# Kernel tuning notes

Hardware: AMD Instinct MI355X
Metric: run time of the kernel (lower is better)

Reference implementation:

```python
import jax, jax.numpy as jnp
import numpy as np

HEADS = 8
EPS = 1e-5


def _layernorm(x, g, b):
    mu = jnp.mean(x, axis=-1, keepdims=True)
    var = jnp.mean(jnp.square(x - mu), axis=-1, keepdims=True)
    return (x - mu) * jax.lax.rsqrt(var + EPS) * g + b


def setup_inputs() -> dict:
    key = jax.random.key(0)
    ks = jax.random.split(key, 10)
    B, S, D = 4, 2048, 256
    d_ff = 2 * D
    s = 0.02
    return {
        "x": jax.random.normal(ks[0], (B, S, D), dtype=jnp.float32),
        "ln1_g": jnp.ones((D,), jnp.float32),
        "ln1_b": jnp.zeros((D,), jnp.float32),
        "w_qkv": jax.random.normal(ks[1], (3 * D, D), jnp.float32) * s,
        "b_qkv": jnp.zeros((3 * D,), jnp.float32),
        "w_proj": jax.random.normal(ks[2], (D, D), jnp.float32) * s,
        "b_proj": jnp.zeros((D,), jnp.float32),
        "ln2_g": jnp.ones((D,), jnp.float32),
        "ln2_b": jnp.zeros((D,), jnp.float32),
        "w1": jax.random.normal(ks[3], (d_ff, D), jnp.float32) * s,
        "b1": jnp.zeros((d_ff,), jnp.float32),
        "w2": jax.random.normal(ks[4], (D, d_ff), jnp.float32) * s,
        "b2": jnp.zeros((D,), jnp.float32),
    }


def reference(x, ln1_g, ln1_b, w_qkv, b_qkv, w_proj, b_proj,
              ln2_g, ln2_b, w1, b1, w2, b2):
    B, S, D = x.shape
    H = HEADS
    dh = D // H
    scale = dh ** -0.5

    # --- attention sublayer (pre-LN) ---
    y = _layernorm(x, ln1_g, ln1_b)
    qkv = y @ w_qkv.T + b_qkv                       # [B,S,3D]
    qkv = qkv.reshape(B, S, 3, H, dh)
    q = jnp.transpose(qkv[:, :, 0], (0, 2, 1, 3))   # [B,H,S,dh]
    k = jnp.transpose(qkv[:, :, 1], (0, 2, 1, 3))
    v = jnp.transpose(qkv[:, :, 2], (0, 2, 1, 3))
    attn = jax.nn.softmax(jnp.einsum('bhsd,bhtd->bhst', q, k) * scale, axis=-1)
    ctx = jnp.einsum('bhst,bhtd->bhsd', attn, v)    # [B,H,S,dh]
    ctx = jnp.transpose(ctx, (0, 2, 1, 3)).reshape(B, S, D)
    x = x + ctx @ w_proj.T + b_proj

    # --- FFN sublayer (pre-LN) ---
    y = _layernorm(x, ln2_g, ln2_b)
    h = jax.nn.silu(y @ w1.T + b1)                  # [B,S,2D]
    x = x + h @ w2.T + b2
    return x
```

## Files before the change

### kernel.cpp

```cpp
#include <hip/hip_runtime.h>
#include <cstddef>

constexpr int kB   = 4;
constexpr int kS   = 2048;
constexpr int kD   = 256;
constexpr int kH   = 8;
constexpr int kDH  = 32;
constexpr int kDFF = 512;
constexpr int kM   = kB * kS;
constexpr float kEps = 1e-5f;
constexpr float kScaleL2E = 0.17677669529663687f * 1.4426950408889634f;

typedef float f32x4  __attribute__((ext_vector_type(4)));
typedef short bf16x8 __attribute__((ext_vector_type(8)));
typedef unsigned short u16;
typedef unsigned int   u32;

__device__ inline u16 f2bf(float x) {
    union { float f; unsigned u; } c; c.f = x;
    const unsigned r = c.u + 0x7fffu + ((c.u >> 16) & 1u);
    return (u16)(r >> 16);
}

__device__ inline u32 pk_trunc(float lo, float hi) {
    union { float f; u32 u; } a, b; a.f = lo; b.f = hi;
    return __builtin_amdgcn_perm(b.u, a.u, 0x07060302u);
}

__global__ __launch_bounds__(256)
void ln_kernel(const float* __restrict__ x, const float* __restrict__ g,
               const float* __restrict__ b, u16* __restrict__ y)
{
    const int wave = threadIdx.x >> 6;
    const int lane = threadIdx.x & 63;
    const int row  = blockIdx.x * 4 + wave;
    const float4 v = *(const float4*)&x[(size_t)row * kD + lane * 4];
    float s1 = (v.x + v.y) + (v.z + v.w);
    float s2 = (v.x * v.x + v.y * v.y) + (v.z * v.z + v.w * v.w);
    #pragma unroll
    for (int off = 1; off < 64; off <<= 1) {
        s1 += __shfl_xor(s1, off);
        s2 += __shfl_xor(s2, off);
    }
    const float mu  = s1 * (1.0f / kD);
    const float var = s2 * (1.0f / kD) - mu * mu;
    const float inv = rsqrtf(var + kEps);
    const float4 g4 = *(const float4*)&g[lane * 4];
    const float4 b4 = *(const float4*)&b[lane * 4];
    *(ushort4*)&y[(size_t)row * kD + lane * 4] = make_ushort4(
        f2bf((v.x - mu) * inv * g4.x + b4.x),
        f2bf((v.y - mu) * inv * g4.y + b4.y),
        f2bf((v.z - mu) * inv * g4.z + b4.z),
        f2bf((v.w - mu) * inv * g4.w + b4.w));
}

template<int NT, int OUTMODE, bool RES, int KTOT>
__global__ __launch_bounds__(256)
void gemm_bf16(const u16* __restrict__ A, const float* __restrict__ Wf,
               const float* __restrict__ bias, const float* __restrict__ res,
               float* __restrict__ Cf, u16* __restrict__ Cb,
               u16* __restrict__ KbP, u16* __restrict__ VtP, int N)
{
    constexpr int BSTR = KTOT + 4;
    __shared__ u16 Bs[NT * BSTR];
    const int tid  = threadIdx.x;
    const int wave = tid >> 6;
    const int lane = tid & 63;
    const int quad = lane >> 4;
    const int l16  = lane & 15;
    const int m0 = blockIdx.x * 128;
    const int n0 = blockIdx.y * NT;

    {
        constexpr int ITS = (NT * KTOT) / 1024;
        #pragma unroll
        for (int it = 0; it < ITS; ++it) {
            const int e   = it * 1024 + tid * 4;
            const int row = e / KTOT;
            const int col = e & (KTOT - 1);
            const float4 wv = *(const float4*)&Wf[(size_t)(n0 + row) * KTOT + col];
            *(ushort4*)&Bs[row * BSTR + col] = make_ushort4(
                f2bf(wv.x), f2bf(wv.y), f2bf(wv.z), f2bf(wv.w));
        }
    }
    __syncthreads();

    f32x4 acc[2][NT / 16];
    #pragma unroll
    for (int mt = 0; mt < 2; ++mt)
        #pragma unroll
        for (int ni = 0; ni < NT / 16; ++ni) acc[mt][ni] = {0.f, 0.f, 0.f, 0.f};

    const u16* arow0 = &A[(size_t)(m0 + wave * 16 + l16) * KTOT];
    const u16* arow1 = &A[(size_t)(m0 + 64 + wave * 16 + l16) * KTOT];
    #pragma unroll 4
    for (int k0 = 0; k0 < KTOT; k0 += 32) {
        const bf16x8 a0 = *(const bf16x8*)&arow0[k0 + quad * 8];
        const bf16x8 a1 = *(const bf16x8*)&arow1[k0 + quad * 8];
        #pragma unroll
        for (int ni = 0; ni < NT / 16; ++ni) {
            const bf16x8 bf = *(const bf16x8*)&Bs[(ni * 16 + l16) * BSTR + k0 + quad * 8];
            acc[0][ni] = __builtin_amdgcn_mfma_f32_16x16x32_bf16(a0, bf, acc[0][ni], 0, 0, 0);
            acc[1][ni] = __builtin_amdgcn_mfma_f32_16x16x32_bf16(a1, bf, acc[1][ni], 0, 0, 0);
        }
    }

    #pragma unroll
    for (int mt = 0; mt < 2; ++mt) {
        #pragma unroll
        for (int ni = 0; ni < NT / 16; ++ni) {
            const float bias_v = bias[n0 + ni * 16 + l16];
            #pragma unroll
            for (int r = 0; r < 4; ++r) {
                const int m = m0 + mt * 64 + wave * 16 + quad * 4 + r;
                float v = acc[mt][ni][r] + bias_v;
                if (OUTMODE == 0) {
                    const int n = n0 + ni * 16 + l16;
                    if (RES) v += res[(size_t)m * N + n];
                    Cf[(size_t)m * N + n] = v;
                } else if (OUTMODE == 1) {
                    const int n = n0 + ni * 16 + l16;
                    v = v / (1.0f + __expf(-v));
                    Cb[(size_t)m * N + n] = f2bf(v);
                } else {
                    const int rgn = n0 >> 8;
                    const int nl  = (n0 & 255) + ni * 16 + l16;
                    const int hh  = nl >> 5, dh = nl & 31;
                    const int bb  = m >> 11, s = m & (kS - 1);
                    const int bh  = bb * kH + hh;
                    if (rgn == 0)
                        Cb[((size_t)bh * kS + s) * kDH + dh] = f2bf(v * kScaleL2E);
                    else if (rgn == 1)
                        KbP[((size_t)bh * kS + s) * kDH + dh] = f2bf(v);
                    else {
                        const int so = s & 31;
                        const int vq = (so >> 2) & 3;
                        const int vj = (so & 3) | (((so >> 4) & 1) << 2);
                        VtP[(((size_t)bh * (kS / 32) + (s >> 5)) * 4 + vq) * 256
                            + dh * 8 + vj] = f2bf(v);
                    }
                }
            }
        }
    }
}

__global__ __launch_bounds__(256)
void attn_kernel(const u16* __restrict__ Qb, const u16* __restrict__ Kb,
                 const u16* __restrict__ Vp, u16* __restrict__ ctx)
{
    __shared__ float cbuf[2][32 * 33];
    const int tid  = threadIdx.x;
    const int wave = tid >> 6;
    const int lane = tid & 63;
    const int quad = lane >> 4;
    const int l16  = lane & 15;
    const int h = blockIdx.y;
    const int b = blockIdx.z;
    const int bh = b * kH + h;
    const int qsub = wave >> 1;
    const int half = wave & 1;
    const int q0 = blockIdx.x * 64 + qsub * 32;

    bf16x8 aq[2];
    aq[0] = *(const bf16x8*)&Qb[((size_t)bh * kS + q0 + l16) * kDH + quad * 8];
    aq[1] = *(const bf16x8*)&Qb[((size_t)bh * kS + q0 + 16 + l16) * kDH + quad * 8];

    const u16* Kbase = Kb + (size_t)bh * kS * kDH;
    const u16* Vbase = Vp + (size_t)bh * (kS * 32);

    f32x4 O[2][2] = {};
    float lp[2] = {0.f, 0.f};
    const f32x4 zz = {0.f, 0.f, 0.f, 0.f};

    const int kbeg = half * (kS / 2);
    #pragma unroll 1
    for (int kt = kbeg; kt < kbeg + kS / 2; kt += 64) {
        bf16x8 kf[4];
        #pragma unroll
        for (int kg = 0; kg < 4; ++kg)
            kf[kg] = *(const bf16x8*)
                &Kbase[(size_t)(kt + kg * 16 + l16) * kDH + quad * 8];
        bf16x8 vf[2][2];
        #pragma unroll
        for (int ks = 0; ks < 2; ++ks)
            #pragma unroll
            for (int nf = 0; nf < 2; ++nf)
                vf[ks][nf] = *(const bf16x8*)
                    &Vbase[(size_t)(((kt >> 5) + ks) * 4 + quad) * 1024
                           + (nf * 16 + l16) * 8];

        #pragma unroll
        for (int qb = 0; qb < 2; ++qb) {
            f32x4 S[4];
            #pragma unroll
            for (int kg = 0; kg < 4; ++kg)
                S[kg] = __builtin_amdgcn_mfma_f32_16x16x32_bf16(kf[kg], aq[qb], zz, 0, 0, 0);

            float e0[8], e1[8];
            #pragma unroll
            for (int r = 0; r < 4; ++r) {
                e0[r]     = __builtin_amdgcn_exp2f(S[0][r]);
                e0[4 + r] = __builtin_amdgcn_exp2f(S[1][r]);
                e1[r]     = __builtin_amdgcn_exp2f(S[2][r]);
                e1[4 + r] = __builtin_amdgcn_exp2f(S[3][r]);
            }
            lp[qb] += ((e0[0] + e0[1]) + (e0[2] + e0[3]))
                    + ((e0[4] + e0[5]) + (e0[6] + e0[7]))
                    + ((e1[0] + e1[1]) + (e1[2] + e1[3]))
                    + ((e1[4] + e1[5]) + (e1[6] + e1[7]));
            union { u32 u[4]; bf16x8 v; } pA0, pA1;
            pA0.u[0] = pk_trunc(e0[0], e0[1]);
            pA0.u[1] = pk_trunc(e0[2], e0[3]);
            pA0.u[2] = pk_trunc(e0[4], e0[5]);
            pA0.u[3] = pk_trunc(e0[6], e0[7]);
            pA1.u[0] = pk_trunc(e1[0], e1[1]);
            pA1.u[1] = pk_trunc(e1[2], e1[3]);
            pA1.u[2] = pk_trunc(e1[4], e1[5]);
            pA1.u[3] = pk_trunc(e1[6], e1[7]);

            O[qb][0] = __builtin_amdgcn_mfma_f32_16x16x32_bf16(pA0.v, vf[0][0], O[qb][0], 0, 0, 0);
            O[qb][1] = __builtin_amdgcn_mfma_f32_16x16x32_bf16(pA0.v, vf[0][1], O[qb][1], 0, 0, 0);
            O[qb][0] = __builtin_amdgcn_mfma_f32_16x16x32_bf16(pA1.v, vf[1][0], O[qb][0], 0, 0, 0);
            O[qb][1] = __builtin_amdgcn_mfma_f32_16x16x32_bf16(pA1.v, vf[1][1], O[qb][1], 0, 0, 0);
        }
    }

    #pragma unroll
    for (int qb = 0; qb < 2; ++qb) {
        lp[qb] += __shfl_xor(lp[qb], 16);
        lp[qb] += __shfl_xor(lp[qb], 32);
    }

    float* cb = cbuf[qsub];
    if (half == 1) {
        #pragma unroll
        for (int qb = 0; qb < 2; ++qb)
            #pragma unroll
            for (int r = 0; r < 4; ++r) {
                const int row = qb * 16 + quad * 4 + r;
                cb[row * 33 + l16]      = O[qb][0][r];
                cb[row * 33 + 16 + l16] = O[qb][1][r];
                if (l16 == 0)
                    cb[row * 33 + 32] = __shfl(lp[qb], quad * 4 + r);
            }
    }
    __syncthreads();
    if (half == 0) {
        #pragma unroll
        for (int qb = 0; qb < 2; ++qb)
            #pragma unroll
            for (int r = 0; r < 4; ++r) {
                const int row = qb * 16 + quad * 4 + r;
                const float lq  = __shfl(lp[qb], quad * 4 + r) + cb[row * 33 + 32];
                const float inv = 1.0f / lq;
                const float o0 = O[qb][0][r] + cb[row * 33 + l16];
                const float o1 = O[qb][1][r] + cb[row * 33 + 16 + l16];
                const int q = q0 + row;
                u16* crow = ctx + ((size_t)(b * kS + q)) * kD + h * kDH;
                crow[l16]      = f2bf(o0 * inv);
                crow[16 + l16] = f2bf(o1 * inv);
            }
    }
}

extern "C" void kernel_launch(void* const* d_in, const int* in_sizes, int n_in,
                              void* d_out, int out_size, void* d_ws, size_t ws_size,
                              hipStream_t stream)
{
    const float* x      = (const float*)d_in[0];
    const float* ln1_g  = (const float*)d_in[1];
    const float* ln1_b  = (const float*)d_in[2];
    const float* w_qkv  = (const float*)d_in[3];
    const float* b_qkv  = (const float*)d_in[4];
    const float* w_proj = (const float*)d_in[5];
    const float* b_proj = (const float*)d_in[6];
    const float* ln2_g  = (const float*)d_in[7];
    const float* ln2_b  = (const float*)d_in[8];
    const float* w1     = (const float*)d_in[9];
    const float* b1     = (const float*)d_in[10];
    const float* w2     = (const float*)d_in[11];
    const float* b2     = (const float*)d_in[12];
    float* out = (float*)d_out;

    char* ws = (char*)d_ws;
    u16* Qb  = (u16*)ws;
    u16* Kb  = (u16*)(ws + ((size_t)4  << 20));
    u16* Vp  = (u16*)(ws + ((size_t)8  << 20));
    u16* ctx = (u16*)(ws + ((size_t)12 << 20));
    u16* y   = (u16*)(ws + ((size_t)16 << 20));
    u16* h   = (u16*)ws;

    const dim3 blk(256);

    ln_kernel<<<dim3(kM / 4), blk, 0, stream>>>(x, ln1_g, ln1_b, y);
    gemm_bf16<64, 2, false, 256><<<dim3(kM / 128, 12), blk, 0, stream>>>(
        y, w_qkv, b_qkv, nullptr, nullptr, Qb, Kb, Vp, 0);
    attn_kernel<<<dim3(kS / 64, kH, kB), blk, 0, stream>>>(Qb, Kb, Vp, ctx);
    gemm_bf16<32, 0, true, 256><<<dim3(kM / 128, kD / 32), blk, 0, stream>>>(
        ctx, w_proj, b_proj, x, out, nullptr, nullptr, nullptr, kD);
    ln_kernel<<<dim3(kM / 4), blk, 0, stream>>>(out, ln2_g, ln2_b, y);
    gemm_bf16<64, 1, false, 256><<<dim3(kM / 128, kDFF / 64), blk, 0, stream>>>(
        y, w1, b1, nullptr, nullptr, h, nullptr, nullptr, kDFF);
    gemm_bf16<32, 0, true, 512><<<dim3(kM / 128, kD / 32), blk, 0, stream>>>(
        h, w2, b2, out, out, nullptr, nullptr, nullptr, kD);
}
```

Baseline: 166.4 us.

## Fuse LayerNorm into the A-operand load of the QKV and FFN1 GEMMs

```diff
diff --git a/kernel.cpp b/kernel.cpp
--- a/kernel.cpp
+++ b/kernel.cpp
@@ -27,37 +27,12 @@
     return __builtin_amdgcn_perm(b.u, a.u, 0x07060302u);
 }
 
+template<int NT, int OUTMODE, bool RES, int KTOT, bool LNA>
 __global__ __launch_bounds__(256)
-void ln_kernel(const float* __restrict__ x, const float* __restrict__ g,
-               const float* __restrict__ b, u16* __restrict__ y)
-{
-    const int wave = threadIdx.x >> 6;
-    const int lane = threadIdx.x & 63;
-    const int row  = blockIdx.x * 4 + wave;
-    const float4 v = *(const float4*)&x[(size_t)row * kD + lane * 4];
-    float s1 = (v.x + v.y) + (v.z + v.w);
-    float s2 = (v.x * v.x + v.y * v.y) + (v.z * v.z + v.w * v.w);
-    #pragma unroll
-    for (int off = 1; off < 64; off <<= 1) {
-        s1 += __shfl_xor(s1, off);
-        s2 += __shfl_xor(s2, off);
-    }
-    const float mu  = s1 * (1.0f / kD);
-    const float var = s2 * (1.0f / kD) - mu * mu;
-    const float inv = rsqrtf(var + kEps);
-    const float4 g4 = *(const float4*)&g[lane * 4];
-    const float4 b4 = *(const float4*)&b[lane * 4];
-    *(ushort4*)&y[(size_t)row * kD + lane * 4] = make_ushort4(
-        f2bf((v.x - mu) * inv * g4.x + b4.x),
-        f2bf((v.y - mu) * inv * g4.y + b4.y),
-        f2bf((v.z - mu) * inv * g4.z + b4.z),
-        f2bf((v.w - mu) * inv * g4.w + b4.w));
-}
-
-template<int NT, int OUTMODE, bool RES, int KTOT>
-__global__ __launch_bounds__(256)
-void gemm_bf16(const u16* __restrict__ A, const float* __restrict__ Wf,
-               const float* __restrict__ bias, const float* __restrict__ res,
+void gemm_bf16(const void* __restrict__ Ain, const float* __restrict__ Wf,
+               const float* __restrict__ bias,
+               const float* __restrict__ lng, const float* __restrict__ lnb,
+               const float* __restrict__ res,
                float* __restrict__ Cf, u16* __restrict__ Cb,
                u16* __restrict__ KbP, u16* __restrict__ VtP, int N)
 {
@@ -83,6 +58,56 @@
                 f2bf(wv.x), f2bf(wv.y), f2bf(wv.z), f2bf(wv.w));
         }
     }
+
+    bf16x8 areg[2][LNA ? KTOT / 32 : 1];
+    if constexpr (LNA) {
+        static_assert(KTOT == 256, "LNA assumes K == D == 256");
+        const float* Af = (const float*)Ain;
+        #pragma unroll
+        for (int mt = 0; mt < 2; ++mt) {
+            const float* arow = &Af[(size_t)(m0 + mt * 64 + wave * 16 + l16) * kD];
+            float s1 = 0.f, s2 = 0.f;
+            #pragma unroll
+            for (int t = 0; t < 8; ++t) {
+                const float4 a0 = *(const float4*)&arow[t * 32 + quad * 8];
+                const float4 a1 = *(const float4*)&arow[t * 32 + quad * 8 + 4];
+                s1 += ((a0.x + a0.y) + (a0.z + a0.w))
+                    + ((a1.x + a1.y) + (a1.z + a1.w));
+                s2 = fmaf(a0.x, a0.x, s2); s2 = fmaf(a0.y, a0.y, s2);
+                s2 = fmaf(a0.z, a0.z, s2); s2 = fmaf(a0.w, a0.w, s2);
+                s2 = fmaf(a1.x, a1.x, s2); s2 = fmaf(a1.y, a1.y, s2);
+                s2 = fmaf(a1.z, a1.z, s2); s2 = fmaf(a1.w, a1.w, s2);
+            }
+            s1 += __shfl_xor(s1, 16); s1 += __shfl_xor(s1, 32);
+            s2 += __shfl_xor(s2, 16); s2 += __shfl_xor(s2, 32);
+            const float mu   = s1 * (1.0f / kD);
+            const float rsig = rsqrtf(s2 * (1.0f / kD) - mu * mu + kEps);
+            #pragma unroll
+            for (int t = 0; t < 8; ++t) {
+                const float4 a0 = *(const float4*)&arow[t * 32 + quad * 8];
+                const float4 a1 = *(const float4*)&arow[t * 32 + quad * 8 + 4];
+                const float4 g0 = *(const float4*)&lng[t * 32 + quad * 8];
+                const float4 g1 = *(const float4*)&lng[t * 32 + quad * 8 + 4];
+                const float4 b0 = *(const float4*)&lnb[t * 32 + quad * 8];
+                const float4 b1 = *(const float4*)&lnb[t * 32 + quad * 8 + 4];
+                float e[8];
+                e[0] = fmaf((a0.x - mu) * rsig, g0.x, b0.x);
+                e[1] = fmaf((a0.y - mu) * rsig, g0.y, b0.y);
+                e[2] = fmaf((a0.z - mu) * rsig, g0.z, b0.z);
+                e[3] = fmaf((a0.w - mu) * rsig, g0.w, b0.w);
+                e[4] = fmaf((a1.x - mu) * rsig, g1.x, b1.x);
+                e[5] = fmaf((a1.y - mu) * rsig, g1.y, b1.y);
+                e[6] = fmaf((a1.z - mu) * rsig, g1.z, b1.z);
+                e[7] = fmaf((a1.w - mu) * rsig, g1.w, b1.w);
+                union { u32 u[4]; bf16x8 v; } P;
+                P.u[0] = pk_trunc(e[0], e[1]);
+                P.u[1] = pk_trunc(e[2], e[3]);
+                P.u[2] = pk_trunc(e[4], e[5]);
+                P.u[3] = pk_trunc(e[6], e[7]);
+                areg[mt][t] = P.v;
+            }
+        }
+    }
     __syncthreads();
 
     f32x4 acc[2][NT / 16];
@@ -91,12 +116,18 @@
         #pragma unroll
         for (int ni = 0; ni < NT / 16; ++ni) acc[mt][ni] = {0.f, 0.f, 0.f, 0.f};
 
-    const u16* arow0 = &A[(size_t)(m0 + wave * 16 + l16) * KTOT];
-    const u16* arow1 = &A[(size_t)(m0 + 64 + wave * 16 + l16) * KTOT];
+    const u16* arow0 = LNA ? nullptr : &((const u16*)Ain)[(size_t)(m0 + wave * 16 + l16) * KTOT];
+    const u16* arow1 = LNA ? nullptr : &((const u16*)Ain)[(size_t)(m0 + 64 + wave * 16 + l16) * KTOT];
     #pragma unroll 4
     for (int k0 = 0; k0 < KTOT; k0 += 32) {
-        const bf16x8 a0 = *(const bf16x8*)&arow0[k0 + quad * 8];
-        const bf16x8 a1 = *(const bf16x8*)&arow1[k0 + quad * 8];
+        bf16x8 a0, a1;
+        if constexpr (LNA) {
+            a0 = areg[0][k0 / 32];
+            a1 = areg[1][k0 / 32];
+        } else {
+            a0 = *(const bf16x8*)&arow0[k0 + quad * 8];
+            a1 = *(const bf16x8*)&arow1[k0 + quad * 8];
+        }
         #pragma unroll
         for (int ni = 0; ni < NT / 16; ++ni) {
             const bf16x8 bf = *(const bf16x8*)&Bs[(ni * 16 + l16) * BSTR + k0 + quad * 8];
@@ -288,20 +319,21 @@
     u16* Kb  = (u16*)(ws + ((size_t)4  << 20));
     u16* Vp  = (u16*)(ws + ((size_t)8  << 20));
     u16* ctx = (u16*)(ws + ((size_t)12 << 20));
-    u16* y   = (u16*)(ws + ((size_t)16 << 20));
     u16* h   = (u16*)ws;
 
     const dim3 blk(256);
 
-    ln_kernel<<<dim3(kM / 4), blk, 0, stream>>>(x, ln1_g, ln1_b, y);
-    gemm_bf16<64, 2, false, 256><<<dim3(kM / 128, 12), blk, 0, stream>>>(
-        y, w_qkv, b_qkv, nullptr, nullptr, Qb, Kb, Vp, 0);
+    gemm_bf16<64, 2, false, 256, true><<<dim3(kM / 128, 12), blk, 0, stream>>>(
+        x, w_qkv, b_qkv, ln1_g, ln1_b, nullptr,
+        nullptr, Qb, Kb, Vp, 0);
     attn_kernel<<<dim3(kS / 64, kH, kB), blk, 0, stream>>>(Qb, Kb, Vp, ctx);
-    gemm_bf16<32, 0, true, 256><<<dim3(kM / 128, kD / 32), blk, 0, stream>>>(
-        ctx, w_proj, b_proj, x, out, nullptr, nullptr, nullptr, kD);
-    ln_kernel<<<dim3(kM / 4), blk, 0, stream>>>(out, ln2_g, ln2_b, y);
-    gemm_bf16<64, 1, false, 256><<<dim3(kM / 128, kDFF / 64), blk, 0, stream>>>(
-        y, w1, b1, nullptr, nullptr, h, nullptr, nullptr, kDFF);
-    gemm_bf16<32, 0, true, 512><<<dim3(kM / 128, kD / 32), blk, 0, stream>>>(
-        h, w2, b2, out, out, nullptr, nullptr, nullptr, kD);
-}
+    gemm_bf16<32, 0, true, 256, false><<<dim3(kM / 128, kD / 32), blk, 0, stream>>>(
+        ctx, w_proj, b_proj, nullptr, nullptr, x,
+        out, nullptr, nullptr, nullptr, kD);
+    gemm_bf16<64, 1, false, 256, true><<<dim3(kM / 128, kDFF / 64), blk, 0, stream>>>(
+        out, w1, b1, ln2_g, ln2_b, nullptr,
+        nullptr, h, nullptr, nullptr, kDFF);
+    gemm_bf16<32, 0, true, 512, false><<<dim3(kM / 128, kD / 32), blk, 0, stream>>>(
+        h, w2, b2, nullptr, nullptr, out,
+        out, nullptr, nullptr, nullptr, kD);
+}
```

After: 267.9 us. 1.61x slower.

## Load GEMM weights directly into registers instead of staging through LDS

Applied to the files above, without the earlier changes.

```diff
diff --git a/kernel.cpp b/kernel.cpp
--- a/kernel.cpp
+++ b/kernel.cpp
@@ -54,61 +54,58 @@
         f2bf((v.w - mu) * inv * g4.w + b4.w));
 }
 
-template<int NT, int OUTMODE, bool RES, int KTOT>
+template<int OUTMODE, bool RES, int KTOT>
 __global__ __launch_bounds__(256)
 void gemm_bf16(const u16* __restrict__ A, const float* __restrict__ Wf,
                const float* __restrict__ bias, const float* __restrict__ res,
                float* __restrict__ Cf, u16* __restrict__ Cb,
                u16* __restrict__ KbP, u16* __restrict__ VtP, int N)
 {
-    constexpr int BSTR = KTOT + 4;
-    __shared__ u16 Bs[NT * BSTR];
     const int tid  = threadIdx.x;
     const int wave = tid >> 6;
     const int lane = tid & 63;
     const int quad = lane >> 4;
     const int l16  = lane & 15;
     const int m0 = blockIdx.x * 128;
-    const int n0 = blockIdx.y * NT;
-
-    {
-        constexpr int ITS = (NT * KTOT) / 1024;
-        #pragma unroll
-        for (int it = 0; it < ITS; ++it) {
-            const int e   = it * 1024 + tid * 4;
-            const int row = e / KTOT;
-            const int col = e & (KTOT - 1);
-            const float4 wv = *(const float4*)&Wf[(size_t)(n0 + row) * KTOT + col];
-            *(ushort4*)&Bs[row * BSTR + col] = make_ushort4(
-                f2bf(wv.x), f2bf(wv.y), f2bf(wv.z), f2bf(wv.w));
-        }
-    }
-    __syncthreads();
-
-    f32x4 acc[2][NT / 16];
-    #pragma unroll
-    for (int mt = 0; mt < 2; ++mt)
-        #pragma unroll
-        for (int ni = 0; ni < NT / 16; ++ni) acc[mt][ni] = {0.f, 0.f, 0.f, 0.f};
+    const int n0 = blockIdx.y * 32;
+
+    f32x4 acc[2][2] = {};
 
     const u16* arow0 = &A[(size_t)(m0 + wave * 16 + l16) * KTOT];
     const u16* arow1 = &A[(size_t)(m0 + 64 + wave * 16 + l16) * KTOT];
-    #pragma unroll 4
-    for (int k0 = 0; k0 < KTOT; k0 += 32) {
-        const bf16x8 a0 = *(const bf16x8*)&arow0[k0 + quad * 8];
-        const bf16x8 a1 = *(const bf16x8*)&arow1[k0 + quad * 8];
-        #pragma unroll
-        for (int ni = 0; ni < NT / 16; ++ni) {
-            const bf16x8 bf = *(const bf16x8*)&Bs[(ni * 16 + l16) * BSTR + k0 + quad * 8];
-            acc[0][ni] = __builtin_amdgcn_mfma_f32_16x16x32_bf16(a0, bf, acc[0][ni], 0, 0, 0);
-            acc[1][ni] = __builtin_amdgcn_mfma_f32_16x16x32_bf16(a1, bf, acc[1][ni], 0, 0, 0);
+
+    #pragma unroll
+    for (int kc = 0; kc < KTOT; kc += 256) {
+        bf16x8 breg[2][8];
+        #pragma unroll
+        for (int ni = 0; ni < 2; ++ni) {
+            const float* wrow = &Wf[(size_t)(n0 + ni * 16 + l16) * KTOT + kc + quad * 8];
+            #pragma unroll
+            for (int t = 0; t < 8; ++t) {
+                const float4 w0 = *(const float4*)&wrow[t * 32];
+                const float4 w1 = *(const float4*)&wrow[t * 32 + 4];
+                union { ushort4 s[2]; bf16x8 v; } P;
+                P.s[0] = make_ushort4(f2bf(w0.x), f2bf(w0.y), f2bf(w0.z), f2bf(w0.w));
+                P.s[1] = make_ushort4(f2bf(w1.x), f2bf(w1.y), f2bf(w1.z), f2bf(w1.w));
+                breg[ni][t] = P.v;
+            }
+        }
+        #pragma unroll
+        for (int t = 0; t < 8; ++t) {
+            const int k0 = kc + t * 32;
+            const bf16x8 a0 = *(const bf16x8*)&arow0[k0 + quad * 8];
+            const bf16x8 a1 = *(const bf16x8*)&arow1[k0 + quad * 8];
+            acc[0][0] = __builtin_amdgcn_mfma_f32_16x16x32_bf16(a0, breg[0][t], acc[0][0], 0, 0, 0);
+            acc[1][0] = __builtin_amdgcn_mfma_f32_16x16x32_bf16(a1, breg[0][t], acc[1][0], 0, 0, 0);
+            acc[0][1] = __builtin_amdgcn_mfma_f32_16x16x32_bf16(a0, breg[1][t], acc[0][1], 0, 0, 0);
+            acc[1][1] = __builtin_amdgcn_mfma_f32_16x16x32_bf16(a1, breg[1][t], acc[1][1], 0, 0, 0);
         }
     }
 
     #pragma unroll
     for (int mt = 0; mt < 2; ++mt) {
         #pragma unroll
-        for (int ni = 0; ni < NT / 16; ++ni) {
+        for (int ni = 0; ni < 2; ++ni) {
             const float bias_v = bias[n0 + ni * 16 + l16];
             #pragma unroll
             for (int r = 0; r < 4; ++r) {
@@ -294,14 +291,14 @@
     const dim3 blk(256);
 
     ln_kernel<<<dim3(kM / 4), blk, 0, stream>>>(x, ln1_g, ln1_b, y);
-    gemm_bf16<64, 2, false, 256><<<dim3(kM / 128, 12), blk, 0, stream>>>(
+    gemm_bf16<2, false, 256><<<dim3(kM / 128, 24), blk, 0, stream>>>(
         y, w_qkv, b_qkv, nullptr, nullptr, Qb, Kb, Vp, 0);
     attn_kernel<<<dim3(kS / 64, kH, kB), blk, 0, stream>>>(Qb, Kb, Vp, ctx);
-    gemm_bf16<32, 0, true, 256><<<dim3(kM / 128, kD / 32), blk, 0, stream>>>(
+    gemm_bf16<0, true, 256><<<dim3(kM / 128, kD / 32), blk, 0, stream>>>(
         ctx, w_proj, b_proj, x, out, nullptr, nullptr, nullptr, kD);
     ln_kernel<<<dim3(kM / 4), blk, 0, stream>>>(out, ln2_g, ln2_b, y);
-    gemm_bf16<64, 1, false, 256><<<dim3(kM / 128, kDFF / 64), blk, 0, stream>>>(
+    gemm_bf16<1, false, 256><<<dim3(kM / 128, kDFF / 32), blk, 0, stream>>>(
         y, w1, b1, nullptr, nullptr, h, nullptr, nullptr, kDFF);
-    gemm_bf16<32, 0, true, 512><<<dim3(kM / 128, kD / 32), blk, 0, stream>>>(
+    gemm_bf16<0, true, 512><<<dim3(kM / 128, kD / 32), blk, 0, stream>>>(
         h, w2, b2, out, out, nullptr, nullptr, nullptr, kD);
 }
```

Result: slower. 216.3 us (+30.0%).

## Retile GEMMs to 256x32 blocks and compute softmax row sums via MFMA

Applied to the files above, without the earlier changes.

```diff
diff --git a/kernel.cpp b/kernel.cpp
--- a/kernel.cpp
+++ b/kernel.cpp
@@ -54,7 +54,7 @@
         f2bf((v.w - mu) * inv * g4.w + b4.w));
 }
 
-template<int NT, int OUTMODE, bool RES, int KTOT>
+template<int OUTMODE, bool RES, int KTOT>
 __global__ __launch_bounds__(256)
 void gemm_bf16(const u16* __restrict__ A, const float* __restrict__ Wf,
                const float* __restrict__ bias, const float* __restrict__ res,
@@ -62,17 +62,17 @@
                u16* __restrict__ KbP, u16* __restrict__ VtP, int N)
 {
     constexpr int BSTR = KTOT + 4;
-    __shared__ u16 Bs[NT * BSTR];
+    __shared__ u16 Bs[32 * BSTR];
     const int tid  = threadIdx.x;
     const int wave = tid >> 6;
     const int lane = tid & 63;
     const int quad = lane >> 4;
     const int l16  = lane & 15;
-    const int m0 = blockIdx.x * 128;
-    const int n0 = blockIdx.y * NT;
+    const int m0 = blockIdx.x * 256;
+    const int n0 = blockIdx.y * 32;
 
     {
-        constexpr int ITS = (NT * KTOT) / 1024;
+        constexpr int ITS = (32 * KTOT) / 1024;
         #pragma unroll
         for (int it = 0; it < ITS; ++it) {
             const int e   = it * 1024 + tid * 4;
@@ -85,30 +85,29 @@
     }
     __syncthreads();
 
-    f32x4 acc[2][NT / 16];
+    f32x4 acc[4][2] = {};
+
+    const u16* arow[4];
     #pragma unroll
-    for (int mt = 0; mt < 2; ++mt)
-        #pragma unroll
-        for (int ni = 0; ni < NT / 16; ++ni) acc[mt][ni] = {0.f, 0.f, 0.f, 0.f};
-
-    const u16* arow0 = &A[(size_t)(m0 + wave * 16 + l16) * KTOT];
-    const u16* arow1 = &A[(size_t)(m0 + 64 + wave * 16 + l16) * KTOT];
+    for (int mt = 0; mt < 4; ++mt)
+        arow[mt] = &A[(size_t)(m0 + mt * 64 + wave * 16 + l16) * KTOT];
+
     #pragma unroll 4
     for (int k0 = 0; k0 < KTOT; k0 += 32) {
-        const bf16x8 a0 = *(const bf16x8*)&arow0[k0 + quad * 8];
-        const bf16x8 a1 = *(const bf16x8*)&arow1[k0 + quad * 8];
-        #pragma unroll
-        for (int ni = 0; ni < NT / 16; ++ni) {
-            const bf16x8 bf = *(const bf16x8*)&Bs[(ni * 16 + l16) * BSTR + k0 + quad * 8];
-            acc[0][ni] = __builtin_amdgcn_mfma_f32_16x16x32_bf16(a0, bf, acc[0][ni], 0, 0, 0);
-            acc[1][ni] = __builtin_amdgcn_mfma_f32_16x16x32_bf16(a1, bf, acc[1][ni], 0, 0, 0);
+        const bf16x8 b0 = *(const bf16x8*)&Bs[l16 * BSTR + k0 + quad * 8];
+        const bf16x8 b1 = *(const bf16x8*)&Bs[(16 + l16) * BSTR + k0 + quad * 8];
+        #pragma unroll
+        for (int mt = 0; mt < 4; ++mt) {
+            const bf16x8 a = *(const bf16x8*)&arow[mt][k0 + quad * 8];
+            acc[mt][0] = __builtin_amdgcn_mfma_f32_16x16x32_bf16(a, b0, acc[mt][0], 0, 0, 0);
+            acc[mt][1] = __builtin_amdgcn_mfma_f32_16x16x32_bf16(a, b1, acc[mt][1], 0, 0, 0);
         }
     }
 
     #pragma unroll
-    for (int mt = 0; mt < 2; ++mt) {
-        #pragma unroll
-        for (int ni = 0; ni < NT / 16; ++ni) {
+    for (int mt = 0; mt < 4; ++mt) {
+        #pragma unroll
+        for (int ni = 0; ni < 2; ++ni) {
             const float bias_v = bias[n0 + ni * 16 + l16];
             #pragma unroll
             for (int r = 0; r < 4; ++r) {
@@ -169,8 +168,12 @@
     const u16* Kbase = Kb + (size_t)bh * kS * kDH;
     const u16* Vbase = Vp + (size_t)bh * (kS * 32);
 
+    bf16x8 ones;
+    #pragma unroll
+    for (int i = 0; i < 8; ++i) ones[i] = (short)0x3F80;
+
     f32x4 O[2][2] = {};
-    float lp[2] = {0.f, 0.f};
+    f32x4 lacc[2] = {};
     const f32x4 zz = {0.f, 0.f, 0.f, 0.f};
 
     const int kbeg = half * (kS / 2);
@@ -205,10 +208,6 @@
                 e1[r]     = __builtin_amdgcn_exp2f(S[2][r]);
                 e1[4 + r] = __builtin_amdgcn_exp2f(S[3][r]);
             }
-            lp[qb] += ((e0[0] + e0[1]) + (e0[2] + e0[3]))
-                    + ((e0[4] + e0[5]) + (e0[6] + e0[7]))
-                    + ((e1[0] + e1[1]) + (e1[2] + e1[3]))
-                    + ((e1[4] + e1[5]) + (e1[6] + e1[7]));
             union { u32 u[4]; bf16x8 v; } pA0, pA1;
             pA0.u[0] = pk_trunc(e0[0], e0[1]);
             pA0.u[1] = pk_trunc(e0[2], e0[3]);
@@ -221,15 +220,11 @@
 
             O[qb][0] = __builtin_amdgcn_mfma_f32_16x16x32_bf16(pA0.v, vf[0][0], O[qb][0], 0, 0, 0);
             O[qb][1] = __builtin_amdgcn_mfma_f32_16x16x32_bf16(pA0.v, vf[0][1], O[qb][1], 0, 0, 0);
+            lacc[qb] = __builtin_amdgcn_mfma_f32_16x16x32_bf16(pA0.v, ones, lacc[qb], 0, 0, 0);
             O[qb][0] = __builtin_amdgcn_mfma_f32_16x16x32_bf16(pA1.v, vf[1][0], O[qb][0], 0, 0, 0);
             O[qb][1] = __builtin_amdgcn_mfma_f32_16x16x32_bf16(pA1.v, vf[1][1], O[qb][1], 0, 0, 0);
+            lacc[qb] = __builtin_amdgcn_mfma_f32_16x16x32_bf16(pA1.v, ones, lacc[qb], 0, 0, 0);
         }
-    }
-
-    #pragma unroll
-    for (int qb = 0; qb < 2; ++qb) {
-        lp[qb] += __shfl_xor(lp[qb], 16);
-        lp[qb] += __shfl_xor(lp[qb], 32);
     }
 
     float* cb = cbuf[qsub];
@@ -241,8 +236,7 @@
                 const int row = qb * 16 + quad * 4 + r;
                 cb[row * 33 + l16]      = O[qb][0][r];
                 cb[row * 33 + 16 + l16] = O[qb][1][r];
-                if (l16 == 0)
-                    cb[row * 33 + 32] = __shfl(lp[qb], quad * 4 + r);
+                if (l16 == 0) cb[row * 33 + 32] = lacc[qb][r];
             }
     }
     __syncthreads();
@@ -252,7 +246,7 @@
             #pragma unroll
             for (int r = 0; r < 4; ++r) {
                 const int row = qb * 16 + quad * 4 + r;
-                const float lq  = __shfl(lp[qb], quad * 4 + r) + cb[row * 33 + 32];
+                const float lq  = lacc[qb][r] + cb[row * 33 + 32];
                 const float inv = 1.0f / lq;
                 const float o0 = O[qb][0][r] + cb[row * 33 + l16];
                 const float o1 = O[qb][1][r] + cb[row * 33 + 16 + l16];
@@ -294,14 +288,14 @@
     const dim3 blk(256);
 
     ln_kernel<<<dim3(kM / 4), blk, 0, stream>>>(x, ln1_g, ln1_b, y);
-    gemm_bf16<64, 2, false, 256><<<dim3(kM / 128, 12), blk, 0, stream>>>(
+    gemm_bf16<2, false, 256><<<dim3(kM / 256, 24), blk, 0, stream>>>(
         y, w_qkv, b_qkv, nullptr, nullptr, Qb, Kb, Vp, 0);
     attn_kernel<<<dim3(kS / 64, kH, kB), blk, 0, stream>>>(Qb, Kb, Vp, ctx);
-    gemm_bf16<32, 0, true, 256><<<dim3(kM / 128, kD / 32), blk, 0, stream>>>(
+    gemm_bf16<0, true, 256><<<dim3(kM / 256, kD / 32), blk, 0, stream>>>(
         ctx, w_proj, b_proj, x, out, nullptr, nullptr, nullptr, kD);
     ln_kernel<<<dim3(kM / 4), blk, 0, stream>>>(out, ln2_g, ln2_b, y);
-    gemm_bf16<64, 1, false, 256><<<dim3(kM / 128, kDFF / 64), blk, 0, stream>>>(
+    gemm_bf16<1, false, 256><<<dim3(kM / 256, kDFF / 32), blk, 0, stream>>>(
         y, w1, b1, nullptr, nullptr, h, nullptr, nullptr, kDFF);
-    gemm_bf16<32, 0, true, 512><<<dim3(kM / 128, kD / 32), blk, 0, stream>>>(
+    gemm_bf16<0, true, 512><<<dim3(kM / 256, kD / 32), blk, 0, stream>>>(
         h, w2, b2, out, out, nullptr, nullptr, nullptr, kD);
 }
```

New measurement: 184.2 us. 1.11x slower.
